# Kernel optimization log

Measured on AMD Instinct MI355X. Metric: run time of the kernel, lower is better.

Reference implementation:

```python
import jax, jax.numpy as jnp
import numpy as np


def setup_inputs() -> dict:
    key = jax.random.key(0)
    kq, kk, kv = jax.random.split(key, 3)
    B, H, S, D = 2, 8, 2048, 64
    Q = jax.random.normal(kq, (B, H, S, D), dtype=jnp.float32)
    K = jax.random.normal(kk, (B, 1, S, D), dtype=jnp.float32)
    V = jax.random.normal(kv, (B, 1, S, D), dtype=jnp.float32)
    return {"Q": Q, "K": K, "V": V}


def reference(Q, K, V):
    # Multi-query attention: K/V have a single shared head.
    D = Q.shape[-1]
    scale = 1.0 / jnp.sqrt(jnp.asarray(D, dtype=Q.dtype))
    Kh = K[:, 0]  # [B, S, D]
    Vh = V[:, 0]  # [B, S, D]
    # scores: [B, H, Sq, Sk]
    scores = jnp.einsum('bhqd,bkd->bhqk', Q, Kh) * scale
    probs = jax.nn.softmax(scores, axis=-1)
    out = jnp.einsum('bhqk,bkd->bhqd', probs, Vh)  # [B, H, S, D]
    return out
```

## Files before the change

kernel.cpp:

```cpp
#include <hip/hip_runtime.h>
#include <hip/hip_bf16.h>
#include <stdint.h>

typedef __attribute__((ext_vector_type(8)))  short    bf16x8;
typedef __attribute__((ext_vector_type(16))) float    f32x16;
typedef __attribute__((ext_vector_type(2)))  float    f32x2;
typedef __attribute__((ext_vector_type(4)))  float    float4v;
typedef __attribute__((ext_vector_type(4)))  unsigned uint4v;
typedef __attribute__((ext_vector_type(2)))  int      int2v;

#define DEVINL static __device__ __forceinline__

#define B_  2
#define H_  8
#define S_  2048
#define D_  64
#define KVB 128
#define NKT (S_ / KVB)

DEVINL unsigned short f2bf(float f) {
  union { float f; unsigned u; } v; v.f = f;
  unsigned r = v.u + 0x7FFFu + ((v.u >> 16) & 1u);
  return (unsigned short)(r >> 16);
}

DEVINL unsigned short bfu(float f) {
  __hip_bfloat16 h = __float2bfloat16(f);
  unsigned short u; __builtin_memcpy(&u, &h, 2); return u;
}

DEVINL unsigned pkcvt(float a, float b) {
  return (unsigned)bfu(a) | ((unsigned)bfu(b) << 16);
}

DEVINL void gload_lds16(const void* g, void* l) {
  __builtin_amdgcn_global_load_lds(
      (const __attribute__((address_space(1))) void*)g,
      (__attribute__((address_space(3))) void*)l, 16, 0, 0);
}

DEVINL bf16x8 frag_from_words(unsigned a, unsigned b, unsigned c, unsigned d) {
  union { unsigned u[4]; bf16x8 v; } x;
  x.u[0] = a; x.u[1] = b; x.u[2] = c; x.u[3] = d;
  return x.v;
}

#define CROW(r, hi) (((r) & 3) + 8 * ((r) >> 2) + 4 * (hi))

__global__ __launch_bounds__(256) void prep_kernel(
    const float* __restrict__ K, const float* __restrict__ V,
    unsigned short* __restrict__ Kb, unsigned short* __restrict__ Vt) {
  const int t = threadIdx.x;
  if (blockIdx.x < 128) {
    const int base = blockIdx.x * 2048 + t * 8;
    const float4v a = *(const float4v*)(K + base);
    const float4v b = *(const float4v*)(K + base + 4);
    uint4v o;
    o.x = (unsigned)f2bf(a.x) | ((unsigned)f2bf(a.y) << 16);
    o.y = (unsigned)f2bf(a.z) | ((unsigned)f2bf(a.w) << 16);
    o.z = (unsigned)f2bf(b.x) | ((unsigned)f2bf(b.y) << 16);
    o.w = (unsigned)f2bf(b.z) | ((unsigned)f2bf(b.w) << 16);
    *(uint4v*)(Kb + base) = o;
  } else {
    __shared__ float Vf[64][65];
    const int vb   = blockIdx.x - 128;
    const int b    = vb >> 5;
    const int sblk = vb & 31;
    const int r = t >> 2, c = t & 3;
    const float* src = V + ((size_t)(b * S_ + sblk * 64 + r)) * 64 + c * 16;
#pragma unroll
    for (int j = 0; j < 4; ++j) {
      float4v x = *(const float4v*)(src + 4 * j);
      Vf[r][c * 16 + 4 * j + 0] = x.x;
      Vf[r][c * 16 + 4 * j + 1] = x.y;
      Vf[r][c * 16 + 4 * j + 2] = x.z;
      Vf[r][c * 16 + 4 * j + 3] = x.w;
    }
    __syncthreads();
    unsigned short o[16];
#pragma unroll
    for (int j = 0; j < 16; ++j) o[j] = f2bf(Vf[c * 16 + j][r]);
    unsigned short* dst = Vt + ((size_t)(b * 64 + r)) * S_ + sblk * 64 + c * 16;
    uint4v w0, w1;
    w0.x = (unsigned)o[0]  | ((unsigned)o[1]  << 16);
    w0.y = (unsigned)o[2]  | ((unsigned)o[3]  << 16);
    w0.z = (unsigned)o[4]  | ((unsigned)o[5]  << 16);
    w0.w = (unsigned)o[6]  | ((unsigned)o[7]  << 16);
    w1.x = (unsigned)o[8]  | ((unsigned)o[9]  << 16);
    w1.y = (unsigned)o[10] | ((unsigned)o[11] << 16);
    w1.z = (unsigned)o[12] | ((unsigned)o[13] << 16);
    w1.w = (unsigned)o[14] | ((unsigned)o[15] << 16);
    *(uint4v*)(dst)     = w0;
    *(uint4v*)(dst + 8) = w1;
  }
}

__global__ __launch_bounds__(256, 2) void attn_kernel(
    const float* __restrict__ Q, const unsigned short* __restrict__ Kb,
    const unsigned short* __restrict__ Vt, float* __restrict__ O) {
  __shared__ __align__(16) unsigned char smem[65536];

  const int bid = blockIdx.x;
  const int b  = bid >> 8;
  const int h  = (bid >> 5) & 7;
  const int qt = bid & 31;

  const int tid  = threadIdx.x;
  const int lane = tid & 63;
  const int wave = tid >> 6;
  const int qg   = wave & 1;
  const int kh   = wave >> 1;
  const int hi   = lane >> 5;
  const int lq   = lane & 31;
  const int l7   = lane & 7;

  const unsigned short* Kbase = Kb + (size_t)b * (S_ * 64);
  const unsigned short* Vbase = Vt + (size_t)b * (64 * S_);

  const float qscale = 0.125f * 1.4426950408889634f;
  const float* qrow = Q + ((size_t)((b * H_ + h) * S_) + (size_t)(qt * 64 + qg * 32 + lq)) * 64;
  bf16x8 qfrag[4];
#pragma unroll
  for (int ks = 0; ks < 4; ++ks) {
    const float* p = qrow + ks * 16 + hi * 8;
    float4v x0 = *(const float4v*)(p);
    float4v x1 = *(const float4v*)(p + 4);
    bf16x8 f;
    f[0] = (short)f2bf(x0.x * qscale); f[1] = (short)f2bf(x0.y * qscale);
    f[2] = (short)f2bf(x0.z * qscale); f[3] = (short)f2bf(x0.w * qscale);
    f[4] = (short)f2bf(x1.x * qscale); f[5] = (short)f2bf(x1.y * qscale);
    f[6] = (short)f2bf(x1.z * qscale); f[7] = (short)f2bf(x1.w * qscale);
    qfrag[ks] = f;
  }

  const int krow = lane >> 3;
  const int kch  = (lane & 7) ^ krow;
  const int vrow = lane >> 4;
  const int vb0  = (lane & 15) ^ vrow;

  const unsigned short* kp  = Kbase + (size_t)(wave * 32 + krow) * 64 + kch * 8;
  const unsigned short* vpA = Vbase + (size_t)(wave * 16 + vrow) * S_ + vb0 * 8;
  const unsigned short* vpB = Vbase + (size_t)(wave * 16 + vrow) * S_ + (vb0 ^ 4) * 8;

  f32x16 acc0, acc1;
#pragma unroll
  for (int r = 0; r < 16; ++r) { acc0[r] = 0.f; acc1[r] = 0.f; }
  float mrun = -__builtin_inff();
  float lrun = 0.f;

#define STAGE(BUF)                                                                       \
  do {                                                                                   \
    _Pragma("unroll")                                                                    \
    for (int i = 0; i < 4; ++i) {                                                        \
      gload_lds16(kp + i * 512,                                                          \
                  smem + (BUF) * 16384 + (wave * 4 + i) * 1024 + lane * 16);             \
      gload_lds16(((i & 1) ? vpB : vpA) + i * 8192,                                      \
                  smem + 32768 + (BUF) * 16384 + (wave * 4 + i) * 1024 + lane * 16);     \
    }                                                                                    \
    kp += 8192; vpA += KVB; vpB += KVB;                                                  \
  } while (0)

  STAGE(0);

  int buf = 0;
  for (int kt = 0; kt < NKT; ++kt) {
    __syncthreads();

    if (kt + 1 < NKT) STAGE(buf ^ 1);

    f32x16 c0, c1;
#pragma unroll
    for (int r = 0; r < 16; ++r) { c0[r] = 0.f; c1[r] = 0.f; }
    const unsigned short* Kt = (const unsigned short*)(smem + buf * 16384);
    __builtin_amdgcn_s_setprio(1);
#pragma unroll
    for (int ks = 0; ks < 4; ++ks) {
      const int ch = (2 * ks + hi) ^ l7;
      const bf16x8 a0 = *(const bf16x8*)(Kt + (kh * 64 + lq) * 64 + ch * 8);
      c0 = __builtin_amdgcn_mfma_f32_32x32x16_bf16(a0, qfrag[ks], c0, 0, 0, 0);
      const bf16x8 a1 = *(const bf16x8*)(Kt + (kh * 64 + 32 + lq) * 64 + ch * 8);
      c1 = __builtin_amdgcn_mfma_f32_32x32x16_bf16(a1, qfrag[ks], c1, 0, 0, 0);
    }
    __builtin_amdgcn_s_setprio(0);

    f32x2 m2 = (f32x2){c0[0], c0[1]};
#pragma unroll
    for (int r = 1; r < 8; ++r)
      m2 = __builtin_elementwise_max(m2, (f32x2){c0[2 * r], c0[2 * r + 1]});
#pragma unroll
    for (int r = 0; r < 8; ++r)
      m2 = __builtin_elementwise_max(m2, (f32x2){c1[2 * r], c1[2 * r + 1]});
    float mx = fmaxf(m2.x, m2.y);
    mx = fmaxf(mx, __shfl_xor(mx, 32));

    if (!__all(mx <= mrun + 8.f)) {
      const float mnew = fmaxf(mrun, mx);
      const float fac  = __builtin_amdgcn_exp2f(mrun - mnew);
#pragma unroll
      for (int r = 0; r < 16; ++r) {
        const float fr = __shfl(fac, CROW(r, hi));
        acc0[r] *= fr; acc1[r] *= fr;
      }
      lrun *= fac;
      mrun = mnew;
    }

#pragma unroll
    for (int r = 0; r < 16; ++r) {
      c0[r] = __builtin_amdgcn_exp2f(c0[r] - mrun);
      c1[r] = __builtin_amdgcn_exp2f(c1[r] - mrun);
    }
    f32x2 ps = (f32x2){0.f, 0.f};
#pragma unroll
    for (int r = 0; r < 8; ++r) {
      ps += (f32x2){c0[2 * r], c0[2 * r + 1]};
      ps += (f32x2){c1[2 * r], c1[2 * r + 1]};
    }
    float psum = ps.x + ps.y;
    psum += __shfl_xor(psum, 32);
    lrun += psum;

    const unsigned short* Vb = (const unsigned short*)(smem + 32768 + buf * 16384);
#pragma unroll
    for (int ks = 0; ks < 4; ++ks) {
      const int e = ks & 1;
      const f32x16 ct = (ks >> 1) ? c1 : c0;
      const unsigned wx0 = pkcvt(ct[8 * e + 0], ct[8 * e + 1]);
      const unsigned wx1 = pkcvt(ct[8 * e + 2], ct[8 * e + 3]);
      const unsigned wy0 = pkcvt(ct[8 * e + 4], ct[8 * e + 5]);
      const unsigned wy1 = pkcvt(ct[8 * e + 6], ct[8 * e + 7]);
      const int2v s02 = __builtin_amdgcn_permlane32_swap((int)wx0, (int)wy0, false, false);
      const int2v s13 = __builtin_amdgcn_permlane32_swap((int)wx1, (int)wy1, false, false);
      const bf16x8 pfrag = frag_from_words((unsigned)s02.x, (unsigned)s13.x,
                                           (unsigned)s02.y, (unsigned)s13.y);
      const int ch = (kh * 8) | ((2 * ks + hi) ^ l7);
      __builtin_amdgcn_s_setprio(1);
      const bf16x8 bv0 = *(const bf16x8*)(Vb + (size_t)lq * 128 + ch * 8);
      acc0 = __builtin_amdgcn_mfma_f32_32x32x16_bf16(pfrag, bv0, acc0, 0, 0, 0);
      const bf16x8 bv1 = *(const bf16x8*)(Vb + (size_t)(32 + lq) * 128 + ch * 8);
      acc1 = __builtin_amdgcn_mfma_f32_32x32x16_bf16(pfrag, bv1, acc1, 0, 0, 0);
      __builtin_amdgcn_s_setprio(0);
    }

    buf ^= 1;
  }

  __syncthreads();
  float* Mbuf = (float*)(smem + 16384);
  float* Lbuf = (float*)(smem + 16384 + 512);
  float* Abuf = (float*)(smem + 32768);
  if (lane < 32) {
    Mbuf[(qg * 2 + kh) * 32 + lane] = mrun;
    Lbuf[(qg * 2 + kh) * 32 + lane] = lrun;
  }
  __syncthreads();
  const float mo = Mbuf[(qg * 2 + (kh ^ 1)) * 32 + lq];
  const float lo = Lbuf[(qg * 2 + (kh ^ 1)) * 32 + lq];
  const float mtot  = fmaxf(mrun, mo);
  const float sself = __builtin_amdgcn_exp2f(mrun - mtot);
  const float ltot  = lrun * sself + lo * __builtin_amdgcn_exp2f(mo - mtot);

  if (kh == 1) {
#pragma unroll
    for (int r = 0; r < 16; ++r) {
      const float sr = __shfl(sself, CROW(r, hi));
      Abuf[qg * 2048 + CROW(r, hi) * 64 + lq]      = acc0[r] * sr;
      Abuf[qg * 2048 + CROW(r, hi) * 64 + 32 + lq] = acc1[r] * sr;
    }
  }
  __syncthreads();
  if (kh == 0) {
    const float linv = 1.f / ltot;
    float* obase = O + ((size_t)((b * H_ + h) * S_) + (size_t)(qt * 64 + qg * 32)) * 64;
#pragma unroll
    for (int r = 0; r < 16; ++r) {
      const float sr = __shfl(sself, CROW(r, hi));
      const float iv = __shfl(linv,  CROW(r, hi));
      const int row  = CROW(r, hi);
      obase[(size_t)row * 64 + lq]      = (acc0[r] * sr + Abuf[qg * 2048 + row * 64 + lq]) * iv;
      obase[(size_t)row * 64 + 32 + lq] = (acc1[r] * sr + Abuf[qg * 2048 + row * 64 + 32 + lq]) * iv;
    }
  }
}

extern "C" void kernel_launch(void* const* d_in, const int* in_sizes, int n_in,
                              void* d_out, int out_size, void* d_ws, size_t ws_size,
                              hipStream_t stream) {
  const float* Q = (const float*)d_in[0];
  const float* K = (const float*)d_in[1];
  const float* V = (const float*)d_in[2];
  float* O = (float*)d_out;

  unsigned short* Kb = (unsigned short*)d_ws;
  unsigned short* Vt = Kb + (size_t)B_ * S_ * 64;

  prep_kernel<<<192, 256, 0, stream>>>(K, V, Kb, Vt);
  attn_kernel<<<B_ * H_ * (S_ / 64), 256, 0, stream>>>(Q, Kb, Vt, O);
}
```

Before: 42.38 us.

## Pre-swizzle K/V into MFMA fragment layout and split KV tile across 8 waves

The prep kernel now writes K and V as bf16 tiles already in the 32x32x16 MFMA operand layout, packed contiguously per 128-key tile. The attention kernel can then stage each tile with flat contiguous LDS loads and read fragments with a simple lane*8 addressing, with no XOR swizzles. Blocks grow to 512 threads (8 waves), so each wave covers 32 keys per tile instead of 64, which halves per-wave score registers and raises parallelism. The final merge now combines four partial softmax states per query group instead of two. The cost is more LDS-based reduction work at the end, and the per-block LDS footprint and occupancy change.

After: 43.33 us. +2.2%, slower.

```diff
diff --git a/kernel.cpp b/kernel.cpp
--- a/kernel.cpp
+++ b/kernel.cpp
@@ -49,55 +49,68 @@
 
 __global__ __launch_bounds__(256) void prep_kernel(
     const float* __restrict__ K, const float* __restrict__ V,
-    unsigned short* __restrict__ Kb, unsigned short* __restrict__ Vt) {
-  const int t = threadIdx.x;
-  if (blockIdx.x < 128) {
-    const int base = blockIdx.x * 2048 + t * 8;
-    const float4v a = *(const float4v*)(K + base);
-    const float4v b = *(const float4v*)(K + base + 4);
-    uint4v o;
-    o.x = (unsigned)f2bf(a.x) | ((unsigned)f2bf(a.y) << 16);
-    o.y = (unsigned)f2bf(a.z) | ((unsigned)f2bf(a.w) << 16);
-    o.z = (unsigned)f2bf(b.x) | ((unsigned)f2bf(b.y) << 16);
-    o.w = (unsigned)f2bf(b.z) | ((unsigned)f2bf(b.w) << 16);
-    *(uint4v*)(Kb + base) = o;
+    unsigned short* __restrict__ KVf) {
+  const int blk = blockIdx.x;
+  const int b  = blk >> 5;
+  const int kt = (blk >> 1) & 15;
+  const int t  = threadIdx.x;
+  const int w  = t >> 6, l = t & 63;
+  const int lq = l & 31, hi = l >> 5;
+
+  unsigned short* out = KVf + (size_t)(b * 16 + kt) * 16384;
+
+  if ((blk & 1) == 0) {
+#pragma unroll
+    for (int j = 0; j < 4; ++j) {
+      const int fi = w * 4 + j;
+      const int kh = fi >> 2, ks = fi & 3;
+      const float* src = K + ((size_t)(b * 2048 + kt * 128 + kh * 32 + lq)) * 64 + ks * 16 + hi * 8;
+      const float4v x0 = *(const float4v*)(src);
+      const float4v x1 = *(const float4v*)(src + 4);
+      uint4v o;
+      o.x = (unsigned)f2bf(x0.x) | ((unsigned)f2bf(x0.y) << 16);
+      o.y = (unsigned)f2bf(x0.z) | ((unsigned)f2bf(x0.w) << 16);
+      o.z = (unsigned)f2bf(x1.x) | ((unsigned)f2bf(x1.y) << 16);
+      o.w = (unsigned)f2bf(x1.z) | ((unsigned)f2bf(x1.w) << 16);
+      *(uint4v*)(out + fi * 512 + l * 8) = o;
+    }
   } else {
-    __shared__ float Vf[64][65];
-    const int vb   = blockIdx.x - 128;
-    const int b    = vb >> 5;
-    const int sblk = vb & 31;
-    const int r = t >> 2, c = t & 3;
-    const float* src = V + ((size_t)(b * S_ + sblk * 64 + r)) * 64 + c * 16;
+    __shared__ float Vs[128][65];
+#pragma unroll
+    for (int rep = 0; rep < 4; ++rep) {
+      const int row = rep * 32 + (t >> 3);
+      const int col = (t & 7) * 8;
+      const float* src = V + ((size_t)(b * 2048 + kt * 128 + row)) * 64 + col;
+      const float4v y0 = *(const float4v*)(src);
+      const float4v y1 = *(const float4v*)(src + 4);
+      Vs[row][col + 0] = y0.x; Vs[row][col + 1] = y0.y;
+      Vs[row][col + 2] = y0.z; Vs[row][col + 3] = y0.w;
+      Vs[row][col + 4] = y1.x; Vs[row][col + 5] = y1.y;
+      Vs[row][col + 6] = y1.z; Vs[row][col + 7] = y1.w;
+    }
+    __syncthreads();
 #pragma unroll
     for (int j = 0; j < 4; ++j) {
-      float4v x = *(const float4v*)(src + 4 * j);
-      Vf[r][c * 16 + 4 * j + 0] = x.x;
-      Vf[r][c * 16 + 4 * j + 1] = x.y;
-      Vf[r][c * 16 + 4 * j + 2] = x.z;
-      Vf[r][c * 16 + 4 * j + 3] = x.w;
-    }
-    __syncthreads();
-    unsigned short o[16];
-#pragma unroll
-    for (int j = 0; j < 16; ++j) o[j] = f2bf(Vf[c * 16 + j][r]);
-    unsigned short* dst = Vt + ((size_t)(b * 64 + r)) * S_ + sblk * 64 + c * 16;
-    uint4v w0, w1;
-    w0.x = (unsigned)o[0]  | ((unsigned)o[1]  << 16);
-    w0.y = (unsigned)o[2]  | ((unsigned)o[3]  << 16);
-    w0.z = (unsigned)o[4]  | ((unsigned)o[5]  << 16);
-    w0.w = (unsigned)o[6]  | ((unsigned)o[7]  << 16);
-    w1.x = (unsigned)o[8]  | ((unsigned)o[9]  << 16);
-    w1.y = (unsigned)o[10] | ((unsigned)o[11] << 16);
-    w1.z = (unsigned)o[12] | ((unsigned)o[13] << 16);
-    w1.w = (unsigned)o[14] | ((unsigned)o[15] << 16);
-    *(uint4v*)(dst)     = w0;
-    *(uint4v*)(dst + 8) = w1;
-  }
-}
-
-__global__ __launch_bounds__(256, 2) void attn_kernel(
-    const float* __restrict__ Q, const unsigned short* __restrict__ Kb,
-    const unsigned short* __restrict__ Vt, float* __restrict__ O) {
+      const int fj = w * 4 + j;
+      const int kh = fj >> 2, s = (fj >> 1) & 1, nt = fj & 1;
+      const int d  = nt * 32 + lq;
+      const int k0 = kh * 32 + s * 16 + hi * 8;
+      unsigned short o[8];
+#pragma unroll
+      for (int e = 0; e < 8; ++e) o[e] = f2bf(Vs[k0 + e][d]);
+      uint4v wv;
+      wv.x = (unsigned)o[0] | ((unsigned)o[1] << 16);
+      wv.y = (unsigned)o[2] | ((unsigned)o[3] << 16);
+      wv.z = (unsigned)o[4] | ((unsigned)o[5] << 16);
+      wv.w = (unsigned)o[6] | ((unsigned)o[7] << 16);
+      *(uint4v*)(out + (16 + fj) * 512 + l * 8) = wv;
+    }
+  }
+}
+
+__global__ __launch_bounds__(512, 4) void attn_kernel(
+    const float* __restrict__ Q, const unsigned short* __restrict__ KVf,
+    float* __restrict__ O) {
   __shared__ __align__(16) unsigned char smem[65536];
 
   const int bid = blockIdx.x;
@@ -112,10 +125,8 @@
   const int kh   = wave >> 1;
   const int hi   = lane >> 5;
   const int lq   = lane & 31;
-  const int l7   = lane & 7;
-
-  const unsigned short* Kbase = Kb + (size_t)b * (S_ * 64);
-  const unsigned short* Vbase = Vt + (size_t)b * (64 * S_);
+
+  const unsigned char* kp = (const unsigned char*)KVf + (size_t)b * 16 * 32768;
 
   const float qscale = 0.125f * 1.4426950408889634f;
   const float* qrow = Q + ((size_t)((b * H_ + h) * S_) + (size_t)(qt * 64 + qg * 32 + lq)) * 64;
@@ -133,31 +144,19 @@
     qfrag[ks] = f;
   }
 
-  const int krow = lane >> 3;
-  const int kch  = (lane & 7) ^ krow;
-  const int vrow = lane >> 4;
-  const int vb0  = (lane & 15) ^ vrow;
-
-  const unsigned short* kp  = Kbase + (size_t)(wave * 32 + krow) * 64 + kch * 8;
-  const unsigned short* vpA = Vbase + (size_t)(wave * 16 + vrow) * S_ + vb0 * 8;
-  const unsigned short* vpB = Vbase + (size_t)(wave * 16 + vrow) * S_ + (vb0 ^ 4) * 8;
-
   f32x16 acc0, acc1;
 #pragma unroll
   for (int r = 0; r < 16; ++r) { acc0[r] = 0.f; acc1[r] = 0.f; }
   float mrun = -__builtin_inff();
   float lrun = 0.f;
 
-#define STAGE(BUF)                                                                       \
-  do {                                                                                   \
-    _Pragma("unroll")                                                                    \
-    for (int i = 0; i < 4; ++i) {                                                        \
-      gload_lds16(kp + i * 512,                                                          \
-                  smem + (BUF) * 16384 + (wave * 4 + i) * 1024 + lane * 16);             \
-      gload_lds16(((i & 1) ? vpB : vpA) + i * 8192,                                      \
-                  smem + 32768 + (BUF) * 16384 + (wave * 4 + i) * 1024 + lane * 16);     \
-    }                                                                                    \
-    kp += 8192; vpA += KVB; vpB += KVB;                                                  \
+#define STAGE(BUF)                                                        \
+  do {                                                                    \
+    _Pragma("unroll")                                                     \
+    for (int j = 0; j < 4; ++j)                                           \
+      gload_lds16(kp + j * 8192 + tid * 16,                               \
+                  smem + (BUF) * 32768 + j * 8192 + tid * 16);            \
+    kp += 32768;                                                          \
   } while (0)
 
   STAGE(0);
@@ -168,28 +167,22 @@
 
     if (kt + 1 < NKT) STAGE(buf ^ 1);
 
-    f32x16 c0, c1;
-#pragma unroll
-    for (int r = 0; r < 16; ++r) { c0[r] = 0.f; c1[r] = 0.f; }
-    const unsigned short* Kt = (const unsigned short*)(smem + buf * 16384);
+    const unsigned short* Kt = (const unsigned short*)(smem + buf * 32768) + kh * 2048;
+    f32x16 c;
+#pragma unroll
+    for (int r = 0; r < 16; ++r) c[r] = 0.f;
     __builtin_amdgcn_s_setprio(1);
 #pragma unroll
     for (int ks = 0; ks < 4; ++ks) {
-      const int ch = (2 * ks + hi) ^ l7;
-      const bf16x8 a0 = *(const bf16x8*)(Kt + (kh * 64 + lq) * 64 + ch * 8);
-      c0 = __builtin_amdgcn_mfma_f32_32x32x16_bf16(a0, qfrag[ks], c0, 0, 0, 0);
-      const bf16x8 a1 = *(const bf16x8*)(Kt + (kh * 64 + 32 + lq) * 64 + ch * 8);
-      c1 = __builtin_amdgcn_mfma_f32_32x32x16_bf16(a1, qfrag[ks], c1, 0, 0, 0);
+      const bf16x8 a = *(const bf16x8*)(Kt + ks * 512 + lane * 8);
+      c = __builtin_amdgcn_mfma_f32_32x32x16_bf16(a, qfrag[ks], c, 0, 0, 0);
     }
     __builtin_amdgcn_s_setprio(0);
 
-    f32x2 m2 = (f32x2){c0[0], c0[1]};
+    f32x2 m2 = (f32x2){c[0], c[1]};
 #pragma unroll
     for (int r = 1; r < 8; ++r)
-      m2 = __builtin_elementwise_max(m2, (f32x2){c0[2 * r], c0[2 * r + 1]});
-#pragma unroll
-    for (int r = 0; r < 8; ++r)
-      m2 = __builtin_elementwise_max(m2, (f32x2){c1[2 * r], c1[2 * r + 1]});
+      m2 = __builtin_elementwise_max(m2, (f32x2){c[2 * r], c[2 * r + 1]});
     float mx = fmaxf(m2.x, m2.y);
     mx = fmaxf(mx, __shfl_xor(mx, 32));
 
@@ -206,38 +199,29 @@
     }
 
 #pragma unroll
-    for (int r = 0; r < 16; ++r) {
-      c0[r] = __builtin_amdgcn_exp2f(c0[r] - mrun);
-      c1[r] = __builtin_amdgcn_exp2f(c1[r] - mrun);
-    }
+    for (int r = 0; r < 16; ++r) c[r] = __builtin_amdgcn_exp2f(c[r] - mrun);
     f32x2 ps = (f32x2){0.f, 0.f};
 #pragma unroll
-    for (int r = 0; r < 8; ++r) {
-      ps += (f32x2){c0[2 * r], c0[2 * r + 1]};
-      ps += (f32x2){c1[2 * r], c1[2 * r + 1]};
-    }
+    for (int r = 0; r < 8; ++r) ps += (f32x2){c[2 * r], c[2 * r + 1]};
     float psum = ps.x + ps.y;
     psum += __shfl_xor(psum, 32);
     lrun += psum;
 
-    const unsigned short* Vb = (const unsigned short*)(smem + 32768 + buf * 16384);
-#pragma unroll
-    for (int ks = 0; ks < 4; ++ks) {
-      const int e = ks & 1;
-      const f32x16 ct = (ks >> 1) ? c1 : c0;
-      const unsigned wx0 = pkcvt(ct[8 * e + 0], ct[8 * e + 1]);
-      const unsigned wx1 = pkcvt(ct[8 * e + 2], ct[8 * e + 3]);
-      const unsigned wy0 = pkcvt(ct[8 * e + 4], ct[8 * e + 5]);
-      const unsigned wy1 = pkcvt(ct[8 * e + 6], ct[8 * e + 7]);
+    const unsigned short* Vt = (const unsigned short*)(smem + buf * 32768) + 8192 + kh * 2048;
+#pragma unroll
+    for (int s = 0; s < 2; ++s) {
+      const unsigned wx0 = pkcvt(c[8 * s + 0], c[8 * s + 1]);
+      const unsigned wx1 = pkcvt(c[8 * s + 2], c[8 * s + 3]);
+      const unsigned wy0 = pkcvt(c[8 * s + 4], c[8 * s + 5]);
+      const unsigned wy1 = pkcvt(c[8 * s + 6], c[8 * s + 7]);
       const int2v s02 = __builtin_amdgcn_permlane32_swap((int)wx0, (int)wy0, false, false);
       const int2v s13 = __builtin_amdgcn_permlane32_swap((int)wx1, (int)wy1, false, false);
       const bf16x8 pfrag = frag_from_words((unsigned)s02.x, (unsigned)s13.x,
                                            (unsigned)s02.y, (unsigned)s13.y);
-      const int ch = (kh * 8) | ((2 * ks + hi) ^ l7);
       __builtin_amdgcn_s_setprio(1);
-      const bf16x8 bv0 = *(const bf16x8*)(Vb + (size_t)lq * 128 + ch * 8);
+      const bf16x8 bv0 = *(const bf16x8*)(Vt + (s * 2 + 0) * 512 + lane * 8);
       acc0 = __builtin_amdgcn_mfma_f32_32x32x16_bf16(pfrag, bv0, acc0, 0, 0, 0);
-      const bf16x8 bv1 = *(const bf16x8*)(Vb + (size_t)(32 + lq) * 128 + ch * 8);
+      const bf16x8 bv1 = *(const bf16x8*)(Vt + (s * 2 + 1) * 512 + lane * 8);
       acc1 = __builtin_amdgcn_mfma_f32_32x32x16_bf16(pfrag, bv1, acc1, 0, 0, 0);
       __builtin_amdgcn_s_setprio(0);
     }
@@ -246,39 +230,50 @@
   }
 
   __syncthreads();
-  float* Mbuf = (float*)(smem + 16384);
-  float* Lbuf = (float*)(smem + 16384 + 512);
-  float* Abuf = (float*)(smem + 32768);
+  float* Mb = (float*)smem;
+  float* Lb = Mb + 256;
+  float* Ab = Mb + 512;
   if (lane < 32) {
-    Mbuf[(qg * 2 + kh) * 32 + lane] = mrun;
-    Lbuf[(qg * 2 + kh) * 32 + lane] = lrun;
+    Mb[(qg * 4 + kh) * 32 + lane] = mrun;
+    Lb[(qg * 4 + kh) * 32 + lane] = lrun;
   }
   __syncthreads();
-  const float mo = Mbuf[(qg * 2 + (kh ^ 1)) * 32 + lq];
-  const float lo = Lbuf[(qg * 2 + (kh ^ 1)) * 32 + lq];
-  const float mtot  = fmaxf(mrun, mo);
+  const float m0_ = Mb[(qg * 4 + 0) * 32 + lq], l0_ = Lb[(qg * 4 + 0) * 32 + lq];
+  const float m1_ = Mb[(qg * 4 + 1) * 32 + lq], l1_ = Lb[(qg * 4 + 1) * 32 + lq];
+  const float m2_ = Mb[(qg * 4 + 2) * 32 + lq], l2_ = Lb[(qg * 4 + 2) * 32 + lq];
+  const float m3_ = Mb[(qg * 4 + 3) * 32 + lq], l3_ = Lb[(qg * 4 + 3) * 32 + lq];
+  const float mtot = fmaxf(fmaxf(m0_, m1_), fmaxf(m2_, m3_));
+  const float ltot = l0_ * __builtin_amdgcn_exp2f(m0_ - mtot)
+                   + l1_ * __builtin_amdgcn_exp2f(m1_ - mtot)
+                   + l2_ * __builtin_amdgcn_exp2f(m2_ - mtot)
+                   + l3_ * __builtin_amdgcn_exp2f(m3_ - mtot);
   const float sself = __builtin_amdgcn_exp2f(mrun - mtot);
-  const float ltot  = lrun * sself + lo * __builtin_amdgcn_exp2f(mo - mtot);
-
-  if (kh == 1) {
+
+  if (kh > 0) {
+    float* dst = Ab + (size_t)(qg * 3 + (kh - 1)) * 2048;
 #pragma unroll
     for (int r = 0; r < 16; ++r) {
       const float sr = __shfl(sself, CROW(r, hi));
-      Abuf[qg * 2048 + CROW(r, hi) * 64 + lq]      = acc0[r] * sr;
-      Abuf[qg * 2048 + CROW(r, hi) * 64 + 32 + lq] = acc1[r] * sr;
+      dst[CROW(r, hi) * 64 + lq]      = acc0[r] * sr;
+      dst[CROW(r, hi) * 64 + 32 + lq] = acc1[r] * sr;
     }
   }
   __syncthreads();
   if (kh == 0) {
     const float linv = 1.f / ltot;
+    const float* a0 = Ab + (size_t)(qg * 3 + 0) * 2048;
+    const float* a1 = Ab + (size_t)(qg * 3 + 1) * 2048;
+    const float* a2 = Ab + (size_t)(qg * 3 + 2) * 2048;
     float* obase = O + ((size_t)((b * H_ + h) * S_) + (size_t)(qt * 64 + qg * 32)) * 64;
 #pragma unroll
     for (int r = 0; r < 16; ++r) {
       const float sr = __shfl(sself, CROW(r, hi));
       const float iv = __shfl(linv,  CROW(r, hi));
       const int row  = CROW(r, hi);
-      obase[(size_t)row * 64 + lq]      = (acc0[r] * sr + Abuf[qg * 2048 + row * 64 + lq]) * iv;
-      obase[(size_t)row * 64 + 32 + lq] = (acc1[r] * sr + Abuf[qg * 2048 + row * 64 + 32 + lq]) * iv;
+      obase[(size_t)row * 64 + lq] =
+          (acc0[r] * sr + a0[row * 64 + lq] + a1[row * 64 + lq] + a2[row * 64 + lq]) * iv;
+      obase[(size_t)row * 64 + 32 + lq] =
+          (acc1[r] * sr + a0[row * 64 + 32 + lq] + a1[row * 64 + 32 + lq] + a2[row * 64 + 32 + lq]) * iv;
     }
   }
 }
@@ -291,9 +286,8 @@
   const float* V = (const float*)d_in[2];
   float* O = (float*)d_out;
 
-  unsigned short* Kb = (unsigned short*)d_ws;
-  unsigned short* Vt = Kb + (size_t)B_ * S_ * 64;
-
-  prep_kernel<<<192, 256, 0, stream>>>(K, V, Kb, Vt);
-  attn_kernel<<<B_ * H_ * (S_ / 64), 256, 0, stream>>>(Q, Kb, Vt, O);
-}
+  unsigned short* KVf = (unsigned short*)d_ws;
+
+  prep_kernel<<<64, 256, 0, stream>>>(K, V, KVf);
+  attn_kernel<<<B_ * H_ * (S_ / 64), 512, 0, stream>>>(Q, KVf, O);
+}
```
